# Optimization experiments

Measured on AMD Instinct MI355X. Metric: run time of the kernel, lower is better.

Reference implementation:

```python
import jax, jax.numpy as jnp
import numpy as np

B, N_C, N_T = 8, 2048, 2048
D_S, D_F = 2, 1
K = 32
EMB_OBS = 4
H = 64
N_RBF = 16
NUM_BLKS = 6
RBF_GAMMA = 10.0


def _layer_norm(x, g, b):
    m = jnp.mean(x, -1, keepdims=True)
    v = jnp.var(x, -1, keepdims=True)
    return (x - m) * jax.lax.rsqrt(v + 1e-6) * g + b


def setup_inputs() -> dict:
    key = jax.random.key(0)
    ks = jax.random.split(key, 16)
    D_IN = EMB_OBS + D_S + D_F  # obs-flag embed + coords + features = 7
    return {
        "s_ctx": jax.random.normal(ks[0], (B, N_C, D_S)),
        "f_ctx": jax.random.normal(ks[1], (B, N_C, D_F)),
        "s_test": jax.random.normal(ks[2], (B, N_T, D_S)),
        "obs_table": jax.random.normal(ks[3], (2, EMB_OBS)) * 0.1,
        "emb_w0": jax.random.normal(ks[4], (D_IN, 256)) / np.sqrt(D_IN),
        "emb_b0": jnp.zeros((256,)),
        "emb_w1": jax.random.normal(ks[5], (256, 128)) / np.sqrt(256.0),
        "emb_b1": jnp.zeros((128,)),
        "emb_w2": jax.random.normal(ks[6], (128, H)) / np.sqrt(128.0),
        "emb_b2": jnp.zeros((H,)),
        "ln_g": jnp.ones((H,)),
        "ln_b": jnp.zeros((H,)),
        "rbf_centers": jnp.tile(jnp.linspace(0.0, 4.0, N_RBF)[None, :], (NUM_BLKS, 1)),
        "rbf_w": jax.random.normal(ks[7], (NUM_BLKS, N_RBF)) / np.sqrt(N_RBF),
        "rbf_b": jnp.zeros((NUM_BLKS,)),
        "blk_w1": jax.random.normal(ks[8], (NUM_BLKS, 2 * H, 2 * H)) / np.sqrt(2.0 * H),
        "blk_b1": jnp.zeros((NUM_BLKS, 2 * H)),
        "blk_w2": jax.random.normal(ks[9], (NUM_BLKS, 2 * H, H)) / np.sqrt(2.0 * H),
        "blk_b2": jnp.zeros((NUM_BLKS, H)),
        "blk_ln_g": jnp.ones((NUM_BLKS, H)),
        "blk_ln_b": jnp.zeros((NUM_BLKS, H)),
        "head_w0": jax.random.normal(ks[10], (H, 256)) / np.sqrt(float(H)),
        "head_b0": jnp.zeros((256,)),
        "head_w1": jax.random.normal(ks[11], (256, 64)) / np.sqrt(256.0),
        "head_b1": jnp.zeros((64,)),
        "head_w2": jax.random.normal(ks[12], (64, 2)) / np.sqrt(64.0),
        "head_b2": jnp.zeros((2,)),
    }


def reference(s_ctx, f_ctx, s_test, obs_table, emb_w0, emb_b0, emb_w1, emb_b1,
              emb_w2, emb_b2, ln_g, ln_b, rbf_centers, rbf_w, rbf_b,
              blk_w1, blk_b1, blk_w2, blk_b2, blk_ln_g, blk_ln_b,
              head_w0, head_b0, head_w1, head_b1, head_w2, head_b2):
    Bq, N_c = s_ctx.shape[:2]
    N_t = s_test.shape[1]

    # --- embed: obs flag + coords + (zeroed for test) function values ---
    obs_c = jnp.broadcast_to(obs_table[1], (Bq, N_c, EMB_OBS))  # observed = 1
    obs_t = jnp.broadcast_to(obs_table[0], (Bq, N_t, EMB_OBS))  # unobserved = 0
    f_test = jnp.zeros((Bq, N_t, f_ctx.shape[-1]), f_ctx.dtype)
    ctx = jnp.concatenate([obs_c, s_ctx, f_ctx], -1)
    test = jnp.concatenate([obs_t, s_test, f_test], -1)

    def emb(x):
        h = jax.nn.gelu(x @ emb_w0 + emb_b0)
        h = jax.nn.gelu(h @ emb_w1 + emb_b1)
        return h @ emb_w2 + emb_b2

    x_ctx = _layer_norm(emb(ctx), ln_g, ln_b)
    x_test = _layer_norm(emb(test), ln_g, ln_b)

    # --- kNN graph build (queries -> context senders) ---
    def knn(q, s):
        d2 = jnp.sum((q[:, :, None, :] - s[:, None, :, :]) ** 2, -1)  # (B, Nq, Nc)
        neg, idx = jax.lax.top_k(-d2, K)
        return idx, jnp.sqrt(jnp.maximum(-neg, 1e-12))

    idx_cc, d_cc = knn(s_ctx, s_ctx)
    idx_ct, d_ct = knn(s_test, s_ctx)
    off = (jnp.arange(Bq) * N_c)[:, None, None]
    senders = jnp.concatenate([(idx_cc + off).reshape(-1), (idx_ct + off).reshape(-1)])
    edges = jnp.concatenate([d_cc.reshape(-1), d_ct.reshape(-1)])
    nodes = jnp.concatenate([x_ctx.reshape(Bq * N_c, H), x_test.reshape(Bq * N_t, H)], 0)
    n_node = Bq * (N_c + N_t)
    # receivers = repeat(arange(n_node), K): each node owns a contiguous K-edge block
    send2d = senders.reshape(n_node, K)
    e2d = edges.reshape(n_node, K)
    mask2d = jnp.isfinite(e2d)
    e_safe = jnp.where(mask2d, e2d, 0.0)

    # --- RBF-biased message-passing blocks ---
    for l in range(NUM_BLKS):
        feats = jnp.exp(-RBF_GAMMA * (e_safe[..., None] - rbf_centers[l]) ** 2)  # (n_node, K, N_RBF)
        bias = feats @ rbf_w[l] + rbf_b[l]                                       # (n_node, K)
        bias = jnp.where(mask2d, bias, -1e9)
        w = jax.nn.softmax(bias, axis=-1)
        agg = jnp.einsum('nk,nkh->nh', w, nodes[send2d])  # gather senders + weighted sum
        h = jnp.concatenate([nodes, agg], -1)
        h = jax.nn.gelu(h @ blk_w1[l] + blk_b1[l])
        h = h @ blk_w2[l] + blk_b2[l]
        nodes = _layer_norm(nodes + h, blk_ln_g[l], blk_ln_b[l])

    # --- head + diagonal MVN ---
    x_t = nodes[-Bq * N_t:].reshape(Bq, N_t, H)
    h = jax.nn.gelu(x_t @ head_w0 + head_b0)
    h = jax.nn.gelu(h @ head_w1 + head_b1)
    out = h @ head_w2 + head_b2
    mean = out[..., 0]
    std = jax.nn.softplus(out[..., 1]) + 1e-3
    return mean, std
```

## Files before the change

### kernel.cpp

```cpp
#include <hip/hip_runtime.h>
#include <hip/hip_bf16.h>
#include <hip/hip_fp16.h>
#include <math.h>

using bf16 = __hip_bfloat16;

#define N_CTX   2048
#define N_TST   2048
#define NB      8
#define KNN     32
#define HDIM    64
#define NRBF    16
#define N_CTX_NODES (NB * N_CTX)
#define N_NODE      (NB * (N_CTX + N_TST))
#define POOL_CAP 256

typedef __attribute__((ext_vector_type(8))) short short8;
typedef __attribute__((ext_vector_type(4))) float f32x4;

#define SWZ(r, k) ((k) ^ (((r) & 7) << 3))

__device__ __forceinline__ bool is_f32(const void* probe) {
    return ((const unsigned short*)probe)[0] == 0;
}
template<bool F32>
__device__ __forceinline__ float ldT(const void* p, int i) {
    if constexpr (F32) return ((const float*)p)[i];
    else               return __bfloat162float(((const bf16*)p)[i]);
}
__device__ __forceinline__ float ld(const void* p, int i, bool f32) {
    return f32 ? ((const float*)p)[i]
               : __bfloat162float(((const bf16*)p)[i]);
}
__device__ __forceinline__ unsigned short f2b(float x) {
    bf16 h = __float2bfloat16(x); unsigned short u;
    __builtin_memcpy(&u, &h, 2); return u;
}
__device__ __forceinline__ float b2f(unsigned short u) {
    bf16 h; __builtin_memcpy(&h, &u, 2); return __bfloat162float(h);
}
__device__ __forceinline__ unsigned short f2h(float x) {
    __half h = __float2half(x); unsigned short u;
    __builtin_memcpy(&u, &h, 2); return u;
}
__device__ __forceinline__ float h2f(unsigned short u) {
    __half h; __builtin_memcpy(&h, &u, 2); return __half2float(h);
}
__device__ __forceinline__ float gelu_tanh(float x) {
    float u = -1.5957691216057308f * (x + 0.044715f * x * x * x);
    return x * __builtin_amdgcn_rcpf(1.0f + __expf(u));
}
__device__ __forceinline__ unsigned long long shfl_u64(unsigned long long v, int src) {
    int lo = __shfl((int)(unsigned)v, src);
    int hi = __shfl((int)(unsigned)(v >> 32), src);
    return ((unsigned long long)(unsigned)hi << 32) | (unsigned)lo;
}

__device__ __forceinline__ void batch_barrier(unsigned* cnt, unsigned target) {
    __syncthreads();
    if (threadIdx.x == 0) {
        __hip_atomic_fetch_add(cnt, 1u, __ATOMIC_RELEASE, __HIP_MEMORY_SCOPE_AGENT);
        unsigned v;
        do {
            v = __hip_atomic_load(cnt, __ATOMIC_ACQUIRE, __HIP_MEMORY_SCOPE_AGENT);
            if (v < target) __builtin_amdgcn_s_sleep(2);
        } while (v < target);
    }
    __syncthreads();
}

template<bool F32>
__device__ __forceinline__ void embed_body(
        const void* s_ctx, const void* f_ctx, const void* s_test, const void* obs,
        const void* w0, const void* b0, const void* w1, const void* b1,
        const void* w2, const void* b2, const void* ln_g, const void* ln_b,
        unsigned short* __restrict__ ctxb, float* __restrict__ testf,
        unsigned short* A, unsigned short* W, unsigned short* H0, unsigned short* W2) {
    int tid = threadIdx.x, w = tid >> 6, l = tid & 63;
    int nb = blockIdx.x * 64;
    bool is_test = (nb >= N_CTX_NODES);
    int loc0 = is_test ? nb - N_CTX_NODES : nb;
    int b = loc0 >> 11;

    for (int idx = tid; idx < 64 * 128; idx += 512) A[idx] = 0;
    for (int idx = tid; idx < 256 * 128; idx += 512) W[idx] = 0;
    __syncthreads();

    {   int nn = tid >> 3, slot = tid & 7;
        if (slot < 7) {
            int loc = loc0 + nn;
            int i = loc & (N_CTX - 1);
            float v;
            if (slot < 4)       v = ldT<F32>(obs, (is_test ? 0 : 1) * 4 + slot);
            else if (slot < 6)  v = is_test ? ldT<F32>(s_test, (b * N_TST + i) * 2 + slot - 4)
                                            : ldT<F32>(s_ctx,  (b * N_CTX + i) * 2 + slot - 4);
            else                v = is_test ? 0.0f : ldT<F32>(f_ctx, b * N_CTX + i);
            A[nn * 128 + SWZ(nn, slot)] = f2b(v);
        }
    }
    for (int idx = tid; idx < 7 * 256; idx += 512) {
        int k = idx >> 8, c = idx & 255;
        W[c * 128 + SWZ(c, k)] = f2b(ldT<F32>(w0, idx));
    }
    __syncthreads();

    {
        int rt = w & 3, co = w >> 2;
        int ra = rt * 16 + (l & 15);
        int kb = (l >> 4) << 3;
        short8 av = *(const short8*)&A[ra * 128 + SWZ(ra, kb)];
        f32x4 acc[8];
        #pragma unroll
        for (int c8 = 0; c8 < 8; ++c8) acc[c8] = (f32x4){0.f, 0.f, 0.f, 0.f};
        #pragma unroll
        for (int c8 = 0; c8 < 8; ++c8) {
            int cb = co * 8 + c8;
            int rb = cb * 16 + (l & 15);
            short8 bv = *(const short8*)&W[rb * 128 + SWZ(rb, kb)];
            acc[c8] = __builtin_amdgcn_mfma_f32_16x16x32_bf16(av, bv, acc[c8], 0, 0, 0);
        }
        #pragma unroll
        for (int c8 = 0; c8 < 8; ++c8) {
            int col = (co * 8 + c8) * 16 + (l & 15);
            float bb = ldT<F32>(b0, col);
            #pragma unroll
            for (int reg = 0; reg < 4; ++reg) {
                int r = rt * 16 + (l >> 4) * 4 + reg;
                H0[r * 256 + SWZ(r, col)] = f2b(gelu_tanh(acc[c8][reg] + bb));
            }
        }
    }
    __syncthreads();

    for (int idx = tid; idx < 256 * 128; idx += 512) {
        int k = idx >> 7, c = idx & 127;
        W[c * 256 + SWZ(c, k)] = f2b(ldT<F32>(w1, idx));
    }
    for (int idx = tid; idx < 128 * 64; idx += 512) {
        int k = idx >> 6, c = idx & 63;
        W2[c * 128 + SWZ(c, k)] = f2b(ldT<F32>(w2, idx));
    }
    __syncthreads();

    {
        int rt = w & 3, cq = w >> 2;
        int ra = rt * 16 + (l & 15);
        f32x4 acc[4];
        #pragma unroll
        for (int c4 = 0; c4 < 4; ++c4) acc[c4] = (f32x4){0.f, 0.f, 0.f, 0.f};
        #pragma unroll
        for (int ks = 0; ks < 8; ++ks) {
            int kb = ks * 32 + ((l >> 4) << 3);
            short8 av = *(const short8*)&H0[ra * 256 + SWZ(ra, kb)];
            #pragma unroll
            for (int c4 = 0; c4 < 4; ++c4) {
                int cb = cq * 4 + c4;
                int rb = cb * 16 + (l & 15);
                short8 bv = *(const short8*)&W[rb * 256 + SWZ(rb, kb)];
                acc[c4] = __builtin_amdgcn_mfma_f32_16x16x32_bf16(av, bv, acc[c4], 0, 0, 0);
            }
        }
        #pragma unroll
        for (int c4 = 0; c4 < 4; ++c4) {
            int col = (cq * 4 + c4) * 16 + (l & 15);
            float bb = ldT<F32>(b1, col);
            #pragma unroll
            for (int reg = 0; reg < 4; ++reg) {
                int r = rt * 16 + (l >> 4) * 4 + reg;
                A[r * 128 + SWZ(r, col)] = f2b(gelu_tanh(acc[c4][reg] + bb));
            }
        }
    }
    __syncthreads();

    if (w < 4) {
        f32x4 a2[4];
        #pragma unroll
        for (int cb = 0; cb < 4; ++cb) a2[cb] = (f32x4){0.f, 0.f, 0.f, 0.f};
        int ra = w * 16 + (l & 15);
        #pragma unroll
        for (int ks = 0; ks < 4; ++ks) {
            int kb = ks * 32 + ((l >> 4) << 3);
            short8 av = *(const short8*)&A[ra * 128 + SWZ(ra, kb)];
            #pragma unroll
            for (int cb = 0; cb < 4; ++cb) {
                int rb = cb * 16 + (l & 15);
                short8 bv = *(const short8*)&W2[rb * 128 + SWZ(rb, kb)];
                a2[cb] = __builtin_amdgcn_mfma_f32_16x16x32_bf16(av, bv, a2[cb], 0, 0, 0);
            }
        }
        int colb = l & 15;
        float g4[4], bb4[4], b24[4];
        #pragma unroll
        for (int cb = 0; cb < 4; ++cb) {
            int col = cb * 16 + colb;
            g4[cb]  = ldT<F32>(ln_g, col);
            bb4[cb] = ldT<F32>(ln_b, col);
            b24[cb] = ldT<F32>(b2,  col);
        }
        #pragma unroll
        for (int reg = 0; reg < 4; ++reg) {
            int r = w * 16 + (l >> 4) * 4 + reg;
            float vv[4]; float s = 0.f, s2 = 0.f;
            #pragma unroll
            for (int cb = 0; cb < 4; ++cb) {
                float v = a2[cb][reg] + b24[cb];
                vv[cb] = v; s += v; s2 += v * v;
            }
            #pragma unroll
            for (int o = 8; o > 0; o >>= 1) { s += __shfl_xor(s, o); s2 += __shfl_xor(s2, o); }
            float m = s / 64.0f;
            float var = s2 / 64.0f - m * m;
            float rs = rsqrtf(var + 1e-6f);
            #pragma unroll
            for (int cb = 0; cb < 4; ++cb) {
                int col = cb * 16 + colb;
                float val = (vv[cb] - m) * rs * g4[cb] + bb4[cb];
                if (is_test) testf[(loc0 + r) * HDIM + col] = val;
                else         ctxb[(size_t)(nb + r) * HDIM + col] = f2b(val);
            }
        }
    }
}

__global__ __launch_bounds__(512)
void embed_kernel(const void* s_ctx, const void* f_ctx, const void* s_test,
                  const void* obs, const void* w0, const void* b0,
                  const void* w1, const void* b1, const void* w2, const void* b2,
                  const void* ln_g, const void* ln_b,
                  unsigned short* __restrict__ ctxb, float* __restrict__ testf,
                  const void* bw1, const void* bw2,
                  unsigned short* __restrict__ w1t, unsigned short* __restrict__ w2t) {
    if (blockIdx.x >= 512) {
        bool f32 = is_f32(ln_g);
        int pb = blockIdx.x - 512;
        int lay = pb >> 3, s = pb & 7, t = threadIdx.x;
        for (int idx = s * 2048 + t; idx < (s + 1) * 2048; idx += 512) {
            int k = idx >> 7, c = idx & 127;
            w1t[lay * 16384 + c * 128 + k] = f2b(ld(bw1, lay * 16384 + idx, f32));
        }
        for (int idx = s * 1024 + t; idx < (s + 1) * 1024; idx += 512) {
            int k = idx >> 6, c = idx & 63;
            w2t[lay * 8192 + c * 128 + k] = f2b(ld(bw2, lay * 8192 + idx, f32));
        }
        return;
    }
    __shared__ unsigned short A[64 * 128];
    __shared__ unsigned short W[256 * 128];
    __shared__ unsigned short H0[64 * 256];
    __shared__ unsigned short W2[64 * 128];
    if (is_f32(ln_g))
        embed_body<true>(s_ctx, f_ctx, s_test, obs, w0, b0, w1, b1, w2, b2,
                         ln_g, ln_b, ctxb, testf, A, W, H0, W2);
    else
        embed_body<false>(s_ctx, f_ctx, s_test, obs, w0, b0, w1, b1, w2, b2,
                          ln_g, ln_b, ctxb, testf, A, W, H0, W2);
}

__global__ __launch_bounds__(512) void knn_kernel(const void* s_ctx, const void* s_test,
                                                  const void* probe,
                                                  unsigned short* __restrict__ knn_idx) {
    bool f32 = is_f32(probe);
    int w = threadIdx.x >> 6, l = threadIdx.x & 63;
    int n = blockIdx.x * 8 + w;
    __shared__ float cx[N_CTX], cy[N_CTX];
    __shared__ unsigned long long pool[8][POOL_CAP];
    __shared__ unsigned pcnt[8];

    bool is_test = (n >= N_CTX_NODES);
    int loc = is_test ? n - N_CTX_NODES : n;
    int b = loc >> 11, q = loc & (N_CTX - 1);

    for (int j = threadIdx.x; j < N_CTX; j += 512) {
        cx[j] = ld(s_ctx, (b * N_CTX + j) * 2 + 0, f32);
        cy[j] = ld(s_ctx, (b * N_CTX + j) * 2 + 1, f32);
    }
    __syncthreads();

    float qx = is_test ? ld(s_test, (b * N_TST + q) * 2 + 0, f32) : cx[q];
    float qy = is_test ? ld(s_test, (b * N_TST + q) * 2 + 1, f32) : cy[q];

    unsigned dbits[32];
    unsigned bmin = 0xFFFFFFFFu;
    #pragma unroll
    for (int i = 0; i < 32; ++i) {
        int j = i * 64 + l;
        float dx = qx - cx[j], dy = qy - cy[j];
        float d2 = __fadd_rn(__fmul_rn(dx, dx), __fmul_rn(dy, dy));
        unsigned ub = __float_as_uint(d2);
        dbits[i] = ub;
        bmin = min(bmin, ub);
    }

    unsigned T = 0;
    #pragma unroll
    for (int bit = 31; bit >= 0; --bit) {
        unsigned trial = T | (1u << bit);
        int c = __popcll(__ballot(bmin < trial));
        if (c < 32) T = trial;
    }

    if (l == 0) pcnt[w] = 0;
    unsigned mycnt = 0;
    #pragma unroll
    for (int i = 0; i < 32; ++i) mycnt += (dbits[i] <= T) ? 1u : 0u;
    unsigned off = atomicAdd(&pcnt[w], mycnt);
    #pragma unroll
    for (int i = 0; i < 32; ++i) {
        if (dbits[i] <= T) {
            if (off < POOL_CAP)
                pool[w][off] = ((unsigned long long)dbits[i] << 32) | (unsigned)(i * 64 + l);
            ++off;
        }
    }
    asm volatile("s_waitcnt lgkmcnt(0)" ::: "memory");
    unsigned M = pcnt[w];
    if (M > POOL_CAP) M = POOL_CAP;

    if (M <= 128) {
        unsigned long long my0 = (l < (int)M) ? pool[w][l] : ~0ull;
        unsigned long long my1 = (64 + l < (int)M) ? pool[w][64 + l] : ~0ull;
        unsigned r0 = 0, r1 = 0;
        unsigned M0 = M < 64 ? M : 64;
        for (unsigned jp = 0; jp < M0; ++jp) {
            unsigned long long v = shfl_u64(my0, (int)jp);
            r0 += (v < my0) ? 1u : 0u;
            r1 += (v < my1) ? 1u : 0u;
        }
        for (unsigned jp = 64; jp < M; ++jp) {
            unsigned long long v = shfl_u64(my1, (int)(jp - 64));
            r0 += (v < my0) ? 1u : 0u;
            r1 += (v < my1) ? 1u : 0u;
        }
        if (l < (int)M && r0 < KNN)
            knn_idx[(size_t)n * KNN + r0] = (unsigned short)(my0 & 0xFFFFu);
        if (64 + l < (int)M && r1 < KNN)
            knn_idx[(size_t)n * KNN + r1] = (unsigned short)(my1 & 0xFFFFu);
    } else {
        for (unsigned m = l; m < M; m += 64) {
            unsigned long long me = pool[w][m];
            unsigned rank = 0;
            for (unsigned jp = 0; jp < M; ++jp)
                rank += (pool[w][jp] < me) ? 1u : 0u;
            if (rank < KNN)
                knn_idx[(size_t)n * KNN + rank] = (unsigned short)(me & 0xFFFFu);
        }
    }
}

__global__ __launch_bounds__(1024, 4)
void mp_coop_kernel(unsigned short* __restrict__ ctxA, unsigned short* __restrict__ ctxB,
                    float* __restrict__ testf,
                    const unsigned short* __restrict__ kidx,
                    unsigned* __restrict__ bar,
                    const unsigned short* __restrict__ w1tg,
                    const unsigned short* __restrict__ w2tg,
                    const void* s_ctx, const void* s_test,
                    const void* rbf_c, const void* rbf_w, const void* rbf_b,
                    const void* b1, const void* b2,
                    const void* lng, const void* lnb) {
    bool f32 = is_f32(lng);
    int tid = threadIdx.x, w = tid >> 6, l = tid & 63;

    int batch = blockIdx.x & 7;
    int slot  = blockIdx.x >> 3;
    bool isctx = (slot < 16);
    int lslot = slot & 15;
    int seg0 = batch * N_CTX + lslot * 128;
    int n0   = (isctx ? 0 : N_CTX_NODES) + seg0;
    int bofs = batch * N_CTX;
    unsigned* cnt = bar + batch * 16;

    __shared__ float          state[128 * 64];
    __shared__ unsigned short A0[128 * 128];
    __shared__ unsigned short h1s[128 * 128];
    __shared__ unsigned short wk_l[128 * 32];
    __shared__ unsigned short kidx_l[128 * 32];
    __shared__ unsigned short d_l[128 * 32];

    for (int idx = tid; idx < 128 * 64; idx += 1024)
        state[idx] = isctx ? b2f(ctxA[(size_t)n0 * 64 + idx]) : testf[(size_t)seg0 * 64 + idx];

    for (int idx = tid; idx < 4096; idx += 1024) {
        int i = idx >> 5, kk = idx & 31;
        int n = n0 + i;
        int q = lslot * 128 + i;
        float qx = isctx ? ld(s_ctx, (bofs + q) * 2 + 0, f32)
                         : ld(s_test, (batch * N_TST + q) * 2 + 0, f32);
        float qy = isctx ? ld(s_ctx, (bofs + q) * 2 + 1, f32)
                         : ld(s_test, (batch * N_TST + q) * 2 + 1, f32);
        int si = (int)kidx[(size_t)n * KNN + kk];
        kidx_l[idx] = (unsigned short)si;
        float dx = qx - ld(s_ctx, (bofs + si) * 2 + 0, f32);
        float dy = qy - ld(s_ctx, (bofs + si) * 2 + 1, f32);
        float d2 = __fadd_rn(__fmul_rn(dx, dx), __fmul_rn(dy, dy));
        d_l[idx] = f2h(sqrtf(fmaxf(d2, 1e-12f)));
    }
    __syncthreads();

    const unsigned short* cur = ctxA;
    unsigned short* nxt = ctxB;

    for (int layer = 0; layer < 6; ++layer) {
        for (int p = 0; p < 4; ++p) {
            int i = w * 8 + p * 2 + (l >> 5);
            int kk = l & 31;
            float d = h2f(d_l[i * 32 + kk]);
            float bias = ld(rbf_b, layer, f32);
            #pragma unroll
            for (int j = 0; j < NRBF; ++j) {
                float c = ld(rbf_c, layer * NRBF + j, f32);
                float u = d - c;
                bias += expf(-10.0f * u * u) * ld(rbf_w, layer * NRBF + j, f32);
            }
            float m = bias;
            #pragma unroll
            for (int o = 16; o > 0; o >>= 1) m = fmaxf(m, __shfl_xor(m, o));
            float e = expf(bias - m), s = e;
            #pragma unroll
            for (int o = 16; o > 0; o >>= 1) s += __shfl_xor(s, o);
            wk_l[i * 32 + kk] = f2h(e / s);
        }
        {
            int m = l & 31, h = l >> 5;
            for (int i = w * 8; i < w * 8 + 8; ++i) {
                A0[i * 128 + SWZ(i, l)] = f2b(state[i * 64 + l]);
                float a0 = 0.f, a1 = 0.f, c0 = 0.f, c1 = 0.f;
                #pragma unroll
                for (int k = 0; k < 16; k += 2) {
                    {
                        int kk = 2 * k + h;
                        int si = (int)kidx_l[i * 32 + kk];
                        unsigned u = *(const unsigned*)(cur + (size_t)(bofs + si) * 64 + 2 * m);
                        float wkv = h2f(wk_l[i * 32 + kk]);
                        a0 += wkv * __uint_as_float(u << 16);
                        a1 += wkv * __uint_as_float(u & 0xFFFF0000u);
                    }
                    {
                        int kk = 2 * (k + 1) + h;
                        int si = (int)kidx_l[i * 32 + kk];
                        unsigned u = *(const unsigned*)(cur + (size_t)(bofs + si) * 64 + 2 * m);
                        float wkv = h2f(wk_l[i * 32 + kk]);
                        c0 += wkv * __uint_as_float(u << 16);
                        c1 += wkv * __uint_as_float(u & 0xFFFF0000u);
                    }
                }
                a0 += c0; a1 += c1;
                a0 += __shfl_xor(a0, 32);
                a1 += __shfl_xor(a1, 32);
                if (h == 0) {
                    unsigned pk = (unsigned)f2b(a0) | ((unsigned)f2b(a1) << 16);
                    *(unsigned*)&A0[i * 128 + SWZ(i, 64 + 2 * m)] = pk;
                }
            }
        }
        __syncthreads();

        {
            const unsigned short* wB = w1tg + layer * 16384;
            f32x4 acc[4];
            #pragma unroll
            for (int c4 = 0; c4 < 4; ++c4) acc[c4] = (f32x4){0.f, 0.f, 0.f, 0.f};
            int ra = (w & 7) * 16 + (l & 15);
            #pragma unroll
            for (int ks = 0; ks < 4; ++ks) {
                int kb = ks * 32 + ((l >> 4) << 3);
                short8 av = *(const short8*)&A0[ra * 128 + SWZ(ra, kb)];
                #pragma unroll
                for (int c4 = 0; c4 < 4; ++c4) {
                    int cb = (w >> 3) * 4 + c4;
                    int rb = cb * 16 + (l & 15);
                    short8 bv = *(const short8*)&wB[rb * 128 + kb];
                    acc[c4] = __builtin_amdgcn_mfma_f32_16x16x32_bf16(av, bv, acc[c4], 0, 0, 0);
                }
            }
            #pragma unroll
            for (int c4 = 0; c4 < 4; ++c4) {
                int col = ((w >> 3) * 4 + c4) * 16 + (l & 15);
                float bb = ld(b1, layer * 128 + col, f32);
                #pragma unroll
                for (int reg = 0; reg < 4; ++reg) {
                    int r = (w & 7) * 16 + (l >> 4) * 4 + reg;
                    h1s[r * 128 + SWZ(r, col)] = f2b(gelu_tanh(acc[c4][reg] + bb));
                }
            }
        }
        __syncthreads();

        if (w < 8) {
            const unsigned short* wB2 = w2tg + layer * 8192;
            f32x4 a2[4];
            #pragma unroll
            for (int cb = 0; cb < 4; ++cb) a2[cb] = (f32x4){0.f, 0.f, 0.f, 0.f};
            int ra = w * 16 + (l & 15);
            #pragma unroll
            for (int ks = 0; ks < 4; ++ks) {
                int kb = ks * 32 + ((l >> 4) << 3);
                short8 av = *(const short8*)&h1s[ra * 128 + SWZ(ra, kb)];
                #pragma unroll
                for (int cb = 0; cb < 4; ++cb) {
                    int rb = cb * 16 + (l & 15);
                    short8 bv = *(const short8*)&wB2[rb * 128 + kb];
                    a2[cb] = __builtin_amdgcn_mfma_f32_16x16x32_bf16(av, bv, a2[cb], 0, 0, 0);
                }
            }
            int colb = l & 15;
            float g4[4], bb4[4], b24[4];
            #pragma unroll
            for (int cb = 0; cb < 4; ++cb) {
                int col = cb * 16 + colb;
                g4[cb]  = ld(lng, layer * 64 + col, f32);
                bb4[cb] = ld(lnb, layer * 64 + col, f32);
                b24[cb] = ld(b2,  layer * 64 + col, f32);
            }
            #pragma unroll
            for (int reg = 0; reg < 4; ++reg) {
                int r = w * 16 + (l >> 4) * 4 + reg;
                float vv[4]; float s = 0.f, s2 = 0.f;
                #pragma unroll
                for (int cb = 0; cb < 4; ++cb) {
                    int col = cb * 16 + colb;
                    float v = a2[cb][reg] + b24[cb] + state[r * 64 + col];
                    vv[cb] = v; s += v; s2 += v * v;
                }
                #pragma unroll
                for (int o = 8; o > 0; o >>= 1) { s += __shfl_xor(s, o); s2 += __shfl_xor(s2, o); }
                float m = s / 64.0f;
                float var = s2 / 64.0f - m * m;
                float rs = rsqrtf(var + 1e-6f);
                #pragma unroll
                for (int cb = 0; cb < 4; ++cb) {
                    int col = cb * 16 + colb;
                    float val = (vv[cb] - m) * rs * g4[cb] + bb4[cb];
                    state[r * 64 + col] = val;
                    if (layer < 5) {
                        if (isctx) nxt[(size_t)(n0 + r) * 64 + col] = f2b(val);
                    } else {
                        if (!isctx) testf[(size_t)(seg0 + r) * 64 + col] = val;
                    }
                }
            }
        }

        if (layer < 5) {
            batch_barrier(cnt, 32u * (unsigned)(layer + 1));
            const unsigned short* t1 = cur; cur = nxt; nxt = (unsigned short*)t1;
        }
    }
}

template<bool F32>
__device__ __forceinline__ void head_body(
        const float* __restrict__ testf, const void* w0, const void* b0,
        const void* w1, const void* b1, const void* w2, const void* b2, void* out,
        float (*xs)[64], float (*h0)[256], float (*h1)[64]) {
    int t = threadIdx.x;
    int pb = blockIdx.x * 16;

    for (int idx = t; idx < 1024; idx += 256)
        xs[idx >> 6][idx & 63] = testf[(pb + (idx >> 6)) * HDIM + (idx & 63)];
    __syncthreads();

    {   float bb = ldT<F32>(b0, t);
        float a[16];
        #pragma unroll
        for (int j = 0; j < 16; ++j) a[j] = bb;
        for (int i = 0; i < 64; ++i) {
            float wv = ldT<F32>(w0, i * 256 + t);
            #pragma unroll
            for (int j = 0; j < 16; ++j) a[j] += xs[j][i] * wv;
        }
        #pragma unroll
        for (int j = 0; j < 16; ++j) h0[j][t] = gelu_tanh(a[j]);
    }
    __syncthreads();

    {   int c = t & 63, g = t >> 6;
        float bb = ldT<F32>(b1, c);
        float a0 = bb, a1 = bb, a2 = bb, a3 = bb;
        for (int i = 0; i < 256; ++i) {
            float wv = ldT<F32>(w1, i * 64 + c);
            a0 += h0[g][i] * wv;      a1 += h0[g + 4][i] * wv;
            a2 += h0[g + 8][i] * wv;  a3 += h0[g + 12][i] * wv;
        }
        h1[g][c]      = gelu_tanh(a0); h1[g + 4][c]  = gelu_tanh(a1);
        h1[g + 8][c]  = gelu_tanh(a2); h1[g + 12][c] = gelu_tanh(a3);
    }
    __syncthreads();

    if (t < 32) {
        int nn = t >> 1, j = t & 1;
        float a = ldT<F32>(b2, j);
        for (int i = 0; i < 64; ++i) a += h1[nn][i] * ldT<F32>(w2, i * 2 + j);
        float r;
        if (j == 0) r = a;
        else        r = fmaxf(a, 0.0f) + log1pf(expf(-fabsf(a))) + 1e-3f;
        int oi = j * 16384 + pb + nn;
        if constexpr (F32) ((float*)out)[oi] = r;
        else               ((bf16*)out)[oi]  = __float2bfloat16(r);
    }
}

__global__ void head_kernel(const float* __restrict__ testf,
                            const void* w0, const void* b0, const void* w1, const void* b1,
                            const void* w2, const void* b2, const void* probe, void* out) {
    __shared__ float xs[16][64];
    __shared__ float h0[16][256];
    __shared__ float h1[16][64];
    if (is_f32(probe)) head_body<true>(testf, w0, b0, w1, b1, w2, b2, out, xs, h0, h1);
    else               head_body<false>(testf, w0, b0, w1, b1, w2, b2, out, xs, h0, h1);
}

extern "C" void kernel_launch(void* const* d_in, const int* in_sizes, int n_in,
                              void* d_out, int out_size, void* d_ws, size_t ws_size,
                              hipStream_t stream) {
    void* s_ctx   = d_in[0];
    void* f_ctx   = d_in[1];
    void* s_test  = d_in[2];
    void* obs     = d_in[3];
    void* emb_w0  = d_in[4];
    void* emb_b0  = d_in[5];
    void* emb_w1  = d_in[6];
    void* emb_b1  = d_in[7];
    void* emb_w2  = d_in[8];
    void* emb_b2  = d_in[9];
    void* ln_g    = d_in[10];
    void* ln_b    = d_in[11];
    void* rbf_c   = d_in[12];
    void* rbf_w   = d_in[13];
    void* rbf_b   = d_in[14];
    void* blk_w1  = d_in[15];
    void* blk_b1  = d_in[16];
    void* blk_w2  = d_in[17];
    void* blk_b2  = d_in[18];
    void* blk_lng = d_in[19];
    void* blk_lnb = d_in[20];
    void* head_w0 = d_in[21];
    void* head_b0 = d_in[22];
    void* head_w1 = d_in[23];
    void* head_b1 = d_in[24];
    void* head_w2 = d_in[25];
    void* head_b2 = d_in[26];

    unsigned short* ctxA  = (unsigned short*)d_ws;
    unsigned short* ctxB  = (unsigned short*)((char*)d_ws + 2097152);
    float*          testf = (float*)((char*)d_ws + 4194304);
    unsigned short* kidx  = (unsigned short*)((char*)d_ws + 8388608);
    unsigned*       bar   = (unsigned*)((char*)d_ws + 10485760);
    unsigned short* w1t   = (unsigned short*)((char*)d_ws + 10486272);
    unsigned short* w2t   = (unsigned short*)((char*)d_ws + 10682880);

    hipMemsetAsync(bar, 0, 8 * 16 * sizeof(unsigned), stream);

    embed_kernel<<<560, 512, 0, stream>>>(s_ctx, f_ctx, s_test, obs,
        emb_w0, emb_b0, emb_w1, emb_b1, emb_w2, emb_b2, ln_g, ln_b, ctxA, testf,
        blk_w1, blk_w2, w1t, w2t);

    knn_kernel<<<N_NODE / 8, 512, 0, stream>>>(s_ctx, s_test, ln_g, kidx);

    void* kargs[] = { &ctxA, &ctxB, &testf, &kidx, &bar, &w1t, &w2t, &s_ctx, &s_test,
                      &rbf_c, &rbf_w, &rbf_b,
                      &blk_b1, &blk_b2, &blk_lng, &blk_lnb };
    hipLaunchCooperativeKernel((void*)mp_coop_kernel, dim3(256), dim3(1024),
                               kargs, 0, stream);

    head_kernel<<<16384 / 16, 256, 0, stream>>>(testf,
        head_w0, head_b0, head_w1, head_b1, head_w2, head_b2, ln_g, d_out);
}
```

Measured before the change: 409.2 us.

## Fuse kNN search into cooperative message-passing kernel and fold barrier reset into embed

The standalone kNN kernel is removed. Each block of the cooperative message-passing kernel now computes the 32 nearest neighbours for its own 128 nodes, using shared memory (context coordinates aliased over A0, candidate pools aliased over h1s). Neighbour indices and distances go straight into shared memory, which removes the global kidx round trip and one launch. The barrier memset is replaced by an extra embed block that zeroes it. In exchange, the kNN work now runs on only 256 blocks with 16 waves each, recomputes distances to avoid register arrays, and gives up the wider parallelism of the old 4096-block kNN launch.

```diff
diff --git a/kernel.cpp b/kernel.cpp
--- a/kernel.cpp
+++ b/kernel.cpp
@@ -13,7 +13,6 @@
 #define NRBF    16
 #define N_CTX_NODES (NB * N_CTX)
 #define N_NODE      (NB * (N_CTX + N_TST))
-#define POOL_CAP 256
 
 typedef __attribute__((ext_vector_type(8))) short short8;
 typedef __attribute__((ext_vector_type(4))) float f32x4;
@@ -230,7 +229,12 @@
                   const void* ln_g, const void* ln_b,
                   unsigned short* __restrict__ ctxb, float* __restrict__ testf,
                   const void* bw1, const void* bw2,
-                  unsigned short* __restrict__ w1t, unsigned short* __restrict__ w2t) {
+                  unsigned short* __restrict__ w1t, unsigned short* __restrict__ w2t,
+                  unsigned* __restrict__ bar) {
+    if (blockIdx.x == 560) {
+        if (threadIdx.x < 128) bar[threadIdx.x] = 0;
+        return;
+    }
     if (blockIdx.x >= 512) {
         bool f32 = is_f32(ln_g);
         int pb = blockIdx.x - 512;
@@ -257,101 +261,9 @@
                           ln_g, ln_b, ctxb, testf, A, W, H0, W2);
 }
 
-__global__ __launch_bounds__(512) void knn_kernel(const void* s_ctx, const void* s_test,
-                                                  const void* probe,
-                                                  unsigned short* __restrict__ knn_idx) {
-    bool f32 = is_f32(probe);
-    int w = threadIdx.x >> 6, l = threadIdx.x & 63;
-    int n = blockIdx.x * 8 + w;
-    __shared__ float cx[N_CTX], cy[N_CTX];
-    __shared__ unsigned long long pool[8][POOL_CAP];
-    __shared__ unsigned pcnt[8];
-
-    bool is_test = (n >= N_CTX_NODES);
-    int loc = is_test ? n - N_CTX_NODES : n;
-    int b = loc >> 11, q = loc & (N_CTX - 1);
-
-    for (int j = threadIdx.x; j < N_CTX; j += 512) {
-        cx[j] = ld(s_ctx, (b * N_CTX + j) * 2 + 0, f32);
-        cy[j] = ld(s_ctx, (b * N_CTX + j) * 2 + 1, f32);
-    }
-    __syncthreads();
-
-    float qx = is_test ? ld(s_test, (b * N_TST + q) * 2 + 0, f32) : cx[q];
-    float qy = is_test ? ld(s_test, (b * N_TST + q) * 2 + 1, f32) : cy[q];
-
-    unsigned dbits[32];
-    unsigned bmin = 0xFFFFFFFFu;
-    #pragma unroll
-    for (int i = 0; i < 32; ++i) {
-        int j = i * 64 + l;
-        float dx = qx - cx[j], dy = qy - cy[j];
-        float d2 = __fadd_rn(__fmul_rn(dx, dx), __fmul_rn(dy, dy));
-        unsigned ub = __float_as_uint(d2);
-        dbits[i] = ub;
-        bmin = min(bmin, ub);
-    }
-
-    unsigned T = 0;
-    #pragma unroll
-    for (int bit = 31; bit >= 0; --bit) {
-        unsigned trial = T | (1u << bit);
-        int c = __popcll(__ballot(bmin < trial));
-        if (c < 32) T = trial;
-    }
-
-    if (l == 0) pcnt[w] = 0;
-    unsigned mycnt = 0;
-    #pragma unroll
-    for (int i = 0; i < 32; ++i) mycnt += (dbits[i] <= T) ? 1u : 0u;
-    unsigned off = atomicAdd(&pcnt[w], mycnt);
-    #pragma unroll
-    for (int i = 0; i < 32; ++i) {
-        if (dbits[i] <= T) {
-            if (off < POOL_CAP)
-                pool[w][off] = ((unsigned long long)dbits[i] << 32) | (unsigned)(i * 64 + l);
-            ++off;
-        }
-    }
-    asm volatile("s_waitcnt lgkmcnt(0)" ::: "memory");
-    unsigned M = pcnt[w];
-    if (M > POOL_CAP) M = POOL_CAP;
-
-    if (M <= 128) {
-        unsigned long long my0 = (l < (int)M) ? pool[w][l] : ~0ull;
-        unsigned long long my1 = (64 + l < (int)M) ? pool[w][64 + l] : ~0ull;
-        unsigned r0 = 0, r1 = 0;
-        unsigned M0 = M < 64 ? M : 64;
-        for (unsigned jp = 0; jp < M0; ++jp) {
-            unsigned long long v = shfl_u64(my0, (int)jp);
-            r0 += (v < my0) ? 1u : 0u;
-            r1 += (v < my1) ? 1u : 0u;
-        }
-        for (unsigned jp = 64; jp < M; ++jp) {
-            unsigned long long v = shfl_u64(my1, (int)(jp - 64));
-            r0 += (v < my0) ? 1u : 0u;
-            r1 += (v < my1) ? 1u : 0u;
-        }
-        if (l < (int)M && r0 < KNN)
-            knn_idx[(size_t)n * KNN + r0] = (unsigned short)(my0 & 0xFFFFu);
-        if (64 + l < (int)M && r1 < KNN)
-            knn_idx[(size_t)n * KNN + r1] = (unsigned short)(my1 & 0xFFFFu);
-    } else {
-        for (unsigned m = l; m < M; m += 64) {
-            unsigned long long me = pool[w][m];
-            unsigned rank = 0;
-            for (unsigned jp = 0; jp < M; ++jp)
-                rank += (pool[w][jp] < me) ? 1u : 0u;
-            if (rank < KNN)
-                knn_idx[(size_t)n * KNN + rank] = (unsigned short)(me & 0xFFFFu);
-        }
-    }
-}
-
 __global__ __launch_bounds__(1024, 4)
 void mp_coop_kernel(unsigned short* __restrict__ ctxA, unsigned short* __restrict__ ctxB,
                     float* __restrict__ testf,
-                    const unsigned short* __restrict__ kidx,
                     unsigned* __restrict__ bar,
                     const unsigned short* __restrict__ w1tg,
                     const unsigned short* __restrict__ w2tg,
@@ -372,29 +284,108 @@
     unsigned* cnt = bar + batch * 16;
 
     __shared__ float          state[128 * 64];
-    __shared__ unsigned short A0[128 * 128];
-    __shared__ unsigned short h1s[128 * 128];
+    __shared__ alignas(16) unsigned short A0[128 * 128];
+    __shared__ alignas(16) unsigned long long poolbuf[16*256];
     __shared__ unsigned short wk_l[128 * 32];
     __shared__ unsigned short kidx_l[128 * 32];
     __shared__ unsigned short d_l[128 * 32];
+    __shared__ unsigned pcnt[16];
+    unsigned short* h1s = (unsigned short*)poolbuf;
+    float* cx = (float*)A0;
+    float* cy = cx + N_CTX;
 
     for (int idx = tid; idx < 128 * 64; idx += 1024)
         state[idx] = isctx ? b2f(ctxA[(size_t)n0 * 64 + idx]) : testf[(size_t)seg0 * 64 + idx];
-
-    for (int idx = tid; idx < 4096; idx += 1024) {
-        int i = idx >> 5, kk = idx & 31;
-        int n = n0 + i;
-        int q = lslot * 128 + i;
-        float qx = isctx ? ld(s_ctx, (bofs + q) * 2 + 0, f32)
-                         : ld(s_test, (batch * N_TST + q) * 2 + 0, f32);
-        float qy = isctx ? ld(s_ctx, (bofs + q) * 2 + 1, f32)
-                         : ld(s_test, (batch * N_TST + q) * 2 + 1, f32);
-        int si = (int)kidx[(size_t)n * KNN + kk];
-        kidx_l[idx] = (unsigned short)si;
-        float dx = qx - ld(s_ctx, (bofs + si) * 2 + 0, f32);
-        float dy = qy - ld(s_ctx, (bofs + si) * 2 + 1, f32);
-        float d2 = __fadd_rn(__fmul_rn(dx, dx), __fmul_rn(dy, dy));
-        d_l[idx] = f2h(sqrtf(fmaxf(d2, 1e-12f)));
+    for (int j = tid; j < N_CTX; j += 1024) {
+        cx[j] = ld(s_ctx, (bofs + j) * 2 + 0, f32);
+        cy[j] = ld(s_ctx, (bofs + j) * 2 + 1, f32);
+    }
+    __syncthreads();
+
+    {
+        unsigned long long* pool = poolbuf + w * 256;
+        for (int qi = 0; qi < 8; ++qi) {
+            int i = w * 8 + qi;
+            int q = lslot * 128 + i;
+            float qx = isctx ? cx[q] : ld(s_test, (batch * N_TST + q) * 2 + 0, f32);
+            float qy = isctx ? cy[q] : ld(s_test, (batch * N_TST + q) * 2 + 1, f32);
+
+            unsigned bmin = 0xFFFFFFFFu;
+            #pragma unroll
+            for (int ii = 0; ii < 32; ++ii) {
+                int j = ii * 64 + l;
+                float dx = qx - cx[j], dy = qy - cy[j];
+                float d2 = __fadd_rn(__fmul_rn(dx, dx), __fmul_rn(dy, dy));
+                bmin = min(bmin, __float_as_uint(d2));
+            }
+            unsigned T = 0;
+            #pragma unroll
+            for (int bit = 31; bit >= 0; --bit) {
+                unsigned trial = T | (1u << bit);
+                int c = __popcll(__ballot(bmin < trial));
+                if (c < 32) T = trial;
+            }
+            unsigned mask = 0;
+            #pragma unroll
+            for (int ii = 0; ii < 32; ++ii) {
+                int j = ii * 64 + l;
+                float dx = qx - cx[j], dy = qy - cy[j];
+                float d2 = __fadd_rn(__fmul_rn(dx, dx), __fmul_rn(dy, dy));
+                if (__float_as_uint(d2) <= T) mask |= 1u << ii;
+            }
+            if (l == 0) pcnt[w] = 0;
+            unsigned off = atomicAdd(&pcnt[w], (unsigned)__popc(mask));
+            #pragma unroll
+            for (int ii = 0; ii < 32; ++ii) {
+                if (mask & (1u << ii)) {
+                    int j = ii * 64 + l;
+                    float dx = qx - cx[j], dy = qy - cy[j];
+                    float d2 = __fadd_rn(__fmul_rn(dx, dx), __fmul_rn(dy, dy));
+                    if (off < 256)
+                        pool[off] = ((unsigned long long)__float_as_uint(d2) << 32) | (unsigned)j;
+                    ++off;
+                }
+            }
+            asm volatile("s_waitcnt lgkmcnt(0)" ::: "memory");
+            unsigned M = pcnt[w];
+            if (M > 256) M = 256;
+
+            if (M <= 128) {
+                unsigned long long my0 = (l < (int)M) ? pool[l] : ~0ull;
+                unsigned long long my1 = (64 + l < (int)M) ? pool[64 + l] : ~0ull;
+                unsigned r0 = 0, r1 = 0;
+                unsigned M0 = M < 64 ? M : 64;
+                for (unsigned jp = 0; jp < M0; ++jp) {
+                    unsigned long long v = shfl_u64(my0, (int)jp);
+                    r0 += (v < my0) ? 1u : 0u;
+                    r1 += (v < my1) ? 1u : 0u;
+                }
+                for (unsigned jp = 64; jp < M; ++jp) {
+                    unsigned long long v = shfl_u64(my1, (int)(jp - 64));
+                    r0 += (v < my0) ? 1u : 0u;
+                    r1 += (v < my1) ? 1u : 0u;
+                }
+                if (l < (int)M && r0 < KNN) {
+                    kidx_l[i * 32 + r0] = (unsigned short)(my0 & 0xFFFFu);
+                    d_l[i * 32 + r0] = f2h(sqrtf(fmaxf(__uint_as_float((unsigned)(my0 >> 32)), 1e-12f)));
+                }
+                if (64 + l < (int)M && r1 < KNN) {
+                    kidx_l[i * 32 + r1] = (unsigned short)(my1 & 0xFFFFu);
+                    d_l[i * 32 + r1] = f2h(sqrtf(fmaxf(__uint_as_float((unsigned)(my1 >> 32)), 1e-12f)));
+                }
+            } else {
+                for (unsigned m = l; m < M; m += 64) {
+                    unsigned long long me = pool[m];
+                    unsigned rank = 0;
+                    for (unsigned jp = 0; jp < M; ++jp)
+                        rank += (pool[jp] < me) ? 1u : 0u;
+                    if (rank < KNN) {
+                        kidx_l[i * 32 + rank] = (unsigned short)(me & 0xFFFFu);
+                        d_l[i * 32 + rank] = f2h(sqrtf(fmaxf(__uint_as_float((unsigned)(me >> 32)), 1e-12f)));
+                    }
+                }
+            }
+        }
     }
     __syncthreads();
 
@@ -645,20 +636,15 @@
     unsigned short* ctxA  = (unsigned short*)d_ws;
     unsigned short* ctxB  = (unsigned short*)((char*)d_ws + 2097152);
     float*          testf = (float*)((char*)d_ws + 4194304);
-    unsigned short* kidx  = (unsigned short*)((char*)d_ws + 8388608);
     unsigned*       bar   = (unsigned*)((char*)d_ws + 10485760);
     unsigned short* w1t   = (unsigned short*)((char*)d_ws + 10486272);
     unsigned short* w2t   = (unsigned short*)((char*)d_ws + 10682880);
 
-    hipMemsetAsync(bar, 0, 8 * 16 * sizeof(unsigned), stream);
-
-    embed_kernel<<<560, 512, 0, stream>>>(s_ctx, f_ctx, s_test, obs,
+    embed_kernel<<<561, 512, 0, stream>>>(s_ctx, f_ctx, s_test, obs,
         emb_w0, emb_b0, emb_w1, emb_b1, emb_w2, emb_b2, ln_g, ln_b, ctxA, testf,
-        blk_w1, blk_w2, w1t, w2t);
-
-    knn_kernel<<<N_NODE / 8, 512, 0, stream>>>(s_ctx, s_test, ln_g, kidx);
-
-    void* kargs[] = { &ctxA, &ctxB, &testf, &kidx, &bar, &w1t, &w2t, &s_ctx, &s_test,
+        blk_w1, blk_w2, w1t, w2t, bar);
+
+    void* kargs[] = { &ctxA, &ctxB, &testf, &bar, &w1t, &w2t, &s_ctx, &s_test,
                       &rbf_c, &rbf_w, &rbf_b,
                       &blk_b1, &blk_b2, &blk_lng, &blk_lnb };
     hipLaunchCooperativeKernel((void*)mp_coop_kernel, dim3(256), dim3(1024),
```

New measurement: 455.3 us. +11.3%, slower.
